# Kernel tuning notes

Hardware: AMD Instinct MI355X
Metric: run time of the kernel (lower is better)

## Reference

```python
import jax, jax.numpy as jnp
import numpy as np

EPS = 1e-12  # torch F.normalize eps


def setup_inputs() -> dict:
    key = jax.random.key(0)
    k1, k2, k3 = jax.random.split(key, 3)
    N, C, H, W, K = 32, 128, 112, 112, 64
    x = jax.random.normal(k1, (N, C, H, W), dtype=jnp.float32)
    conv_w = jax.random.normal(k2, (K, C), dtype=jnp.float32) * 0.05  # 1x1 conv weight, no bias (vladv2=False)
    centroids = jax.random.uniform(k3, (K, C), dtype=jnp.float32)
    return {"x": x, "conv_w": conv_w, "centroids": centroids}


def reference(x, conv_w, centroids):
    N, C = x.shape[:2]
    K = centroids.shape[0]
    xf = x.reshape(N, C, -1)                       # (N, C, S)
    # 1x1 conv == per-pixel linear: (K,C) @ (N,C,S) -> (N,K,S)
    soft_assign = jnp.einsum('kc,ncs->nks', conv_w, xf)
    soft_assign = jax.nn.softmax(soft_assign, axis=1)  # softmax over clusters
    # vlad[n,k,c] = sum_s a[n,k,s] * (x[n,c,s] - cent[k,c])
    vlad = jnp.einsum('nks,ncs->nkc', soft_assign, xf) \
         - soft_assign.sum(axis=-1)[..., None] * centroids[None, :, :]
    # intra-normalize over descriptor dim
    vlad = vlad / jnp.maximum(jnp.linalg.norm(vlad, axis=2, keepdims=True), EPS)
    vlad = vlad.reshape(N, K * C)
    vlad = vlad / jnp.maximum(jnp.linalg.norm(vlad, axis=1, keepdims=True), EPS)
    return vlad
```

## Files before the change

kernel.cpp:

```cpp
#include <hip/hip_runtime.h>

#define NV_N 32
#define NV_C 128
#define NV_K 64
#define NV_S 12544
#define ST 64
#define TILES 14
#define SCHUNK 14
#define XS 72
#define AS 72

typedef short short8 __attribute__((ext_vector_type(8)));
typedef float floatx4 __attribute__((ext_vector_type(4)));

static __device__ __forceinline__ unsigned short f2bf(float f) {
  union { float f; unsigned u; } v; v.f = f;
  unsigned r = v.u + 0x7FFFu + ((v.u >> 16) & 1u);
  return (unsigned short)(r >> 16);
}

static __device__ __forceinline__ short8 pack8(float4 a, float4 b) {
  union { unsigned short us[8]; short8 s; } u;
  u.us[0] = f2bf(a.x); u.us[1] = f2bf(a.y); u.us[2] = f2bf(a.z); u.us[3] = f2bf(a.w);
  u.us[4] = f2bf(b.x); u.us[5] = f2bf(b.y); u.us[6] = f2bf(b.z); u.us[7] = f2bf(b.w);
  return u.s;
}

__global__ __launch_bounds__(256, 2) void netvlad_main(
    const float* __restrict__ x, const float* __restrict__ conv_w,
    float* __restrict__ vlad_ws, float* __restrict__ asum_ws) {
  __shared__ __attribute__((aligned(16))) unsigned short x_lds[2][NV_C * XS];
  __shared__ __attribute__((aligned(16))) unsigned short a_lds[NV_K * AS];
  __shared__ float asum_sh[4][NV_K];

  const int t = threadIdx.x;
  const int n = blockIdx.x / SCHUNK;
  const int chunk = blockIdx.x % SCHUNK;
  const int s_base = chunk * (ST * TILES);
  const int w = t >> 6;
  const int lane = t & 63;
  const int q = lane >> 4;
  const int l = lane & 15;

  const float* __restrict__ xn = x + (size_t)n * NV_C * NV_S;

  short8 wfrag[4][4];
#pragma unroll
  for (int mt = 0; mt < 4; ++mt)
#pragma unroll
    for (int kc = 0; kc < 4; ++kc) {
      const float* wp = conv_w + (mt * 16 + l) * NV_C + kc * 32 + q * 8;
      float4 wa = *(const float4*)wp;
      float4 wb = *(const float4*)(wp + 4);
      wfrag[mt][kc] = pack8(wa, wb);
    }

  floatx4 acc2[4][2];
  float asum_acc[4][4];
#pragma unroll
  for (int mt = 0; mt < 4; ++mt) {
#pragma unroll
    for (int nt = 0; nt < 2; ++nt) acc2[mt][nt] = (floatx4){0.f, 0.f, 0.f, 0.f};
#pragma unroll
    for (int r = 0; r < 4; ++r) asum_acc[mt][r] = 0.f;
  }

  float4 pf[8];

  {
#pragma unroll
    for (int g = 0; g < 4; ++g) {
      int vec2 = t + g * 256; int c = vec2 >> 3; int sv8 = vec2 & 7;
      const float* p = xn + (size_t)c * NV_S + s_base + sv8 * 8;
      pf[2 * g] = *(const float4*)p;
      pf[2 * g + 1] = *(const float4*)(p + 4);
    }
  }

  for (int tt = 0; tt < TILES; ++tt) {
    const int buf = tt & 1;
#pragma unroll
    for (int g = 0; g < 4; ++g) {
      int vec2 = t + g * 256; int c = vec2 >> 3; int sv8 = vec2 & 7;
      *(short8*)&x_lds[buf][c * XS + sv8 * 8] = pack8(pf[2 * g], pf[2 * g + 1]);
    }
    __syncthreads();

    if (tt + 1 < TILES) {
      const int s0n = s_base + (tt + 1) * ST;
#pragma unroll
      for (int g = 0; g < 4; ++g) {
        int vec2 = t + g * 256; int c = vec2 >> 3; int sv8 = vec2 & 7;
        const float* p = xn + (size_t)c * NV_S + s0n + sv8 * 8;
        pf[2 * g] = *(const float4*)p;
        pf[2 * g + 1] = *(const float4*)(p + 4);
      }
    }

    floatx4 acc1[4];
#pragma unroll
    for (int mt = 0; mt < 4; ++mt) acc1[mt] = (floatx4){0.f, 0.f, 0.f, 0.f};
#pragma unroll
    for (int kc = 0; kc < 4; ++kc) {
      short8 bfr;
#pragma unroll
      for (int j = 0; j < 8; ++j)
        bfr[j] = (short)x_lds[buf][(kc * 32 + q * 8 + j) * XS + w * 16 + l];
#pragma unroll
      for (int mt = 0; mt < 4; ++mt)
        acc1[mt] = __builtin_amdgcn_mfma_f32_16x16x32_bf16(wfrag[mt][kc], bfr, acc1[mt], 0, 0, 0);
    }

    {
      float m = -1e30f;
#pragma unroll
      for (int mt = 0; mt < 4; ++mt)
#pragma unroll
        for (int r = 0; r < 4; ++r) m = fmaxf(m, acc1[mt][r]);
      m = fmaxf(m, __shfl_xor(m, 16));
      m = fmaxf(m, __shfl_xor(m, 32));
      float sum = 0.f;
#pragma unroll
      for (int mt = 0; mt < 4; ++mt)
#pragma unroll
        for (int r = 0; r < 4; ++r) {
          float e = __expf(acc1[mt][r] - m);
          acc1[mt][r] = e; sum += e;
        }
      sum += __shfl_xor(sum, 16);
      sum += __shfl_xor(sum, 32);
      const float inv = 1.0f / sum;
#pragma unroll
      for (int mt = 0; mt < 4; ++mt)
#pragma unroll
        for (int r = 0; r < 4; ++r) {
          float a = acc1[mt][r] * inv;
          asum_acc[mt][r] += a;
          a_lds[(mt * 16 + q * 4 + r) * AS + w * 16 + l] = f2bf(a);
        }
    }
    __syncthreads();

#pragma unroll
    for (int sk = 0; sk < 2; ++sk) {
      short8 afr[4];
#pragma unroll
      for (int mt = 0; mt < 4; ++mt)
        afr[mt] = *(const short8*)&a_lds[(mt * 16 + l) * AS + sk * 32 + q * 8];
#pragma unroll
      for (int nt = 0; nt < 2; ++nt) {
        const short8 bfr = *(const short8*)&x_lds[buf][((w * 2 + nt) * 16 + l) * XS + sk * 32 + q * 8];
#pragma unroll
        for (int mt = 0; mt < 4; ++mt)
          acc2[mt][nt] = __builtin_amdgcn_mfma_f32_16x16x32_bf16(afr[mt], bfr, acc2[mt][nt], 0, 0, 0);
      }
    }
  }

#pragma unroll
  for (int mt = 0; mt < 4; ++mt)
#pragma unroll
    for (int r = 0; r < 4; ++r) {
      float v = asum_acc[mt][r];
      v += __shfl_xor(v, 1); v += __shfl_xor(v, 2);
      v += __shfl_xor(v, 4); v += __shfl_xor(v, 8);
      if (l == 0) asum_sh[w][mt * 16 + q * 4 + r] = v;
    }
  __syncthreads();
  if (t < NV_K)
    atomicAdd(asum_ws + (size_t)n * NV_K + t,
              asum_sh[0][t] + asum_sh[1][t] + asum_sh[2][t] + asum_sh[3][t]);

  float* vw = vlad_ws + (size_t)n * (NV_K * NV_C);
#pragma unroll
  for (int mt = 0; mt < 4; ++mt)
#pragma unroll
    for (int nt = 0; nt < 2; ++nt)
#pragma unroll
      for (int r = 0; r < 4; ++r)
        atomicAdd(vw + (mt * 16 + q * 4 + r) * NV_C + (w * 2 + nt) * 16 + l, acc2[mt][nt][r]);
}

__global__ __launch_bounds__(256) void netvlad_finalize(
    const float* __restrict__ vlad_ws, const float* __restrict__ asum_ws,
    const float* __restrict__ cent, float* __restrict__ out) {
  __shared__ float v_lds[NV_K * NV_C];
  __shared__ float red4[256];
  __shared__ float rscale[NV_K];
  __shared__ float gscale_sh;

  const int t = threadIdx.x; const int n = blockIdx.x;
  const float* vw = vlad_ws + (size_t)n * (NV_K * NV_C);

#pragma unroll
  for (int i = 0; i < 8; ++i) {
    int vec = t + i * 256; int k = vec >> 5; int cq = vec & 31;
    float4 ws = *(const float4*)(vw + k * NV_C + cq * 4);
    float4 ce = *(const float4*)(cent + k * NV_C + cq * 4);
    float as = asum_ws[(size_t)n * NV_K + k];
    float4 v;
    v.x = ws.x - as * ce.x; v.y = ws.y - as * ce.y;
    v.z = ws.z - as * ce.z; v.w = ws.w - as * ce.w;
    *(float4*)&v_lds[k * NV_C + cq * 4] = v;
  }
  __syncthreads();

  {
    const int k = t >> 2, part = t & 3;
    const float* row = &v_lds[k * NV_C + part * 32];
    float ss = 0.0f;
#pragma unroll
    for (int c = 0; c < 32; ++c) { float v = row[c]; ss += v * v; }
    red4[t] = ss;
  }
  __syncthreads();
  if (t < NV_K) {
    float ss = red4[t * 4] + red4[t * 4 + 1] + red4[t * 4 + 2] + red4[t * 4 + 3];
    rscale[t] = 1.0f / fmaxf(sqrtf(ss), 1e-12f);
  }
  __syncthreads();

  float gp = 0.0f;
#pragma unroll
  for (int i = 0; i < 8; ++i) {
    int vec = t + i * 256; int k = vec >> 5; int cq = vec & 31;
    float4 v = *(const float4*)&v_lds[k * NV_C + cq * 4];
    float rs = rscale[k];
    gp += (v.x * v.x + v.y * v.y + v.z * v.z + v.w * v.w) * rs * rs;
  }
  red4[t] = gp;
  __syncthreads();
  if (t < 64) {
    float s = red4[t] + red4[t + 64] + red4[t + 128] + red4[t + 192];
#pragma unroll
    for (int o = 32; o > 0; o >>= 1) s += __shfl_down(s, o);
    if (t == 0) gscale_sh = 1.0f / fmaxf(sqrtf(s), 1e-12f);
  }
  __syncthreads();
  const float gs = gscale_sh;

#pragma unroll
  for (int i = 0; i < 8; ++i) {
    int vec = t + i * 256; int k = vec >> 5; int cq = vec & 31;
    float4 v = *(const float4*)&v_lds[k * NV_C + cq * 4];
    const float sc = rscale[k] * gs;
    v.x *= sc; v.y *= sc; v.z *= sc; v.w *= sc;
    *(float4*)(out + (size_t)n * (NV_K * NV_C) + k * NV_C + cq * 4) = v;
  }
}

extern "C" void kernel_launch(void* const* d_in, const int* in_sizes, int n_in,
                              void* d_out, int out_size, void* d_ws, size_t ws_size,
                              hipStream_t stream) {
  (void)in_sizes; (void)n_in; (void)out_size; (void)ws_size;
  const float* x      = (const float*)d_in[0];
  const float* conv_w = (const float*)d_in[1];
  const float* cent   = (const float*)d_in[2];
  float* out = (float*)d_out;

  float* vlad_ws = (float*)d_ws;
  float* asum_ws = vlad_ws + (size_t)NV_N * NV_K * NV_C;
  const size_t zbytes = ((size_t)NV_N * NV_K * NV_C + (size_t)NV_N * NV_K) * sizeof(float);
  hipMemsetAsync(d_ws, 0, zbytes, stream);

  hipLaunchKernelGGL(netvlad_main, dim3(NV_N * SCHUNK), dim3(256), 0, stream,
                     x, conv_w, vlad_ws, asum_ws);
  hipLaunchKernelGGL(netvlad_finalize, dim3(NV_N), dim3(256), 0, stream,
                     vlad_ws, asum_ws, cent, out);
}
```

Baseline: 299.6 us.

## Swizzle x tile in LDS and replace atomics with per-block partials reduced in finalize

The x tile in LDS now uses an XOR-like rotation of 8-element groups by channel, so both MFMA operand reads avoid bank conflicts. Per-chunk global pointers and write offsets are precomputed once instead of each tile. The float atomicAdds into a zeroed workspace are replaced by plain stores of per-block partials, which the finalize kernel sums over the 14 chunks. This also drops the memset. The cost is more workspace traffic in a finalize kernel that runs only 32 blocks.

```diff
diff --git a/kernel.cpp b/kernel.cpp
--- a/kernel.cpp
+++ b/kernel.cpp
@@ -26,9 +26,10 @@
   return u.s;
 }
 
+
 __global__ __launch_bounds__(256, 2) void netvlad_main(
     const float* __restrict__ x, const float* __restrict__ conv_w,
-    float* __restrict__ vlad_ws, float* __restrict__ asum_ws) {
+    float* __restrict__ vlad_part, float* __restrict__ asum_part) {
   __shared__ __attribute__((aligned(16))) unsigned short x_lds[2][NV_C * XS];
   __shared__ __attribute__((aligned(16))) unsigned short a_lds[NV_K * AS];
   __shared__ float asum_sh[4][NV_K];
@@ -65,35 +66,34 @@
     for (int r = 0; r < 4; ++r) asum_acc[mt][r] = 0.f;
   }
 
+  int wroff[4]; const float* gp[4];
+#pragma unroll
+  for (int g = 0; g < 4; ++g) {
+    int vec2 = t + g * 256; int c = vec2 >> 3; int sv8 = vec2 & 7;
+    wroff[g] = c * XS + (((sv8 + (c >> 3)) & 7) << 3);
+    gp[g] = xn + (size_t)c * NV_S + s_base + sv8 * 8;
+  }
+
   float4 pf[8];
-
-  {
-#pragma unroll
-    for (int g = 0; g < 4; ++g) {
-      int vec2 = t + g * 256; int c = vec2 >> 3; int sv8 = vec2 & 7;
-      const float* p = xn + (size_t)c * NV_S + s_base + sv8 * 8;
-      pf[2 * g] = *(const float4*)p;
-      pf[2 * g + 1] = *(const float4*)(p + 4);
-    }
+#pragma unroll
+  for (int g = 0; g < 4; ++g) {
+    pf[2 * g] = *(const float4*)gp[g];
+    pf[2 * g + 1] = *(const float4*)(gp[g] + 4);
   }
 
   for (int tt = 0; tt < TILES; ++tt) {
     const int buf = tt & 1;
 #pragma unroll
-    for (int g = 0; g < 4; ++g) {
-      int vec2 = t + g * 256; int c = vec2 >> 3; int sv8 = vec2 & 7;
-      *(short8*)&x_lds[buf][c * XS + sv8 * 8] = pack8(pf[2 * g], pf[2 * g + 1]);
-    }
+    for (int g = 0; g < 4; ++g)
+      *(short8*)&x_lds[buf][wroff[g]] = pack8(pf[2 * g], pf[2 * g + 1]);
     __syncthreads();
 
     if (tt + 1 < TILES) {
-      const int s0n = s_base + (tt + 1) * ST;
+      const int soff = (tt + 1) * ST;
 #pragma unroll
       for (int g = 0; g < 4; ++g) {
-        int vec2 = t + g * 256; int c = vec2 >> 3; int sv8 = vec2 & 7;
-        const float* p = xn + (size_t)c * NV_S + s0n + sv8 * 8;
-        pf[2 * g] = *(const float4*)p;
-        pf[2 * g + 1] = *(const float4*)(p + 4);
+        pf[2 * g] = *(const float4*)(gp[g] + soff);
+        pf[2 * g + 1] = *(const float4*)(gp[g] + soff + 4);
       }
     }
 
@@ -102,10 +102,11 @@
     for (int mt = 0; mt < 4; ++mt) acc1[mt] = (floatx4){0.f, 0.f, 0.f, 0.f};
 #pragma unroll
     for (int kc = 0; kc < 4; ++kc) {
+      const int gsel = (w * 2 + (l >> 3) + kc * 4 + q) & 7;
       short8 bfr;
 #pragma unroll
       for (int j = 0; j < 8; ++j)
-        bfr[j] = (short)x_lds[buf][(kc * 32 + q * 8 + j) * XS + w * 16 + l];
+        bfr[j] = (short)x_lds[buf][(kc * 32 + q * 8 + j) * XS + (gsel << 3) + (l & 7)];
 #pragma unroll
       for (int mt = 0; mt < 4; ++mt)
         acc1[mt] = __builtin_amdgcn_mfma_f32_16x16x32_bf16(wfrag[mt][kc], bfr, acc1[mt], 0, 0, 0);
@@ -149,7 +150,9 @@
         afr[mt] = *(const short8*)&a_lds[(mt * 16 + l) * AS + sk * 32 + q * 8];
 #pragma unroll
       for (int nt = 0; nt < 2; ++nt) {
-        const short8 bfr = *(const short8*)&x_lds[buf][((w * 2 + nt) * 16 + l) * XS + sk * 32 + q * 8];
+        const int c2 = (w * 2 + nt) * 16 + l;
+        const int gsel2 = (sk * 4 + q + (c2 >> 3)) & 7;
+        const short8 bfr = *(const short8*)&x_lds[buf][c2 * XS + (gsel2 << 3)];
 #pragma unroll
         for (int mt = 0; mt < 4; ++mt)
           acc2[mt][nt] = __builtin_amdgcn_mfma_f32_16x16x32_bf16(afr[mt], bfr, acc2[mt][nt], 0, 0, 0);
@@ -168,39 +171,54 @@
     }
   __syncthreads();
   if (t < NV_K)
-    atomicAdd(asum_ws + (size_t)n * NV_K + t,
-              asum_sh[0][t] + asum_sh[1][t] + asum_sh[2][t] + asum_sh[3][t]);
-
-  float* vw = vlad_ws + (size_t)n * (NV_K * NV_C);
+    asum_part[(size_t)blockIdx.x * NV_K + t] =
+        asum_sh[0][t] + asum_sh[1][t] + asum_sh[2][t] + asum_sh[3][t];
+
+  float* vp = vlad_part + (size_t)blockIdx.x * (NV_K * NV_C);
 #pragma unroll
   for (int mt = 0; mt < 4; ++mt)
 #pragma unroll
     for (int nt = 0; nt < 2; ++nt)
 #pragma unroll
       for (int r = 0; r < 4; ++r)
-        atomicAdd(vw + (mt * 16 + q * 4 + r) * NV_C + (w * 2 + nt) * 16 + l, acc2[mt][nt][r]);
+        vp[(mt * 16 + q * 4 + r) * NV_C + (w * 2 + nt) * 16 + l] = acc2[mt][nt][r];
 }
 
 __global__ __launch_bounds__(256) void netvlad_finalize(
-    const float* __restrict__ vlad_ws, const float* __restrict__ asum_ws,
+    const float* __restrict__ vlad_part, const float* __restrict__ asum_part,
     const float* __restrict__ cent, float* __restrict__ out) {
   __shared__ float v_lds[NV_K * NV_C];
   __shared__ float red4[256];
   __shared__ float rscale[NV_K];
+  __shared__ float asum_tot[NV_K];
   __shared__ float gscale_sh;
 
   const int t = threadIdx.x; const int n = blockIdx.x;
-  const float* vw = vlad_ws + (size_t)n * (NV_K * NV_C);
+  const float* vp = vlad_part + (size_t)n * SCHUNK * (NV_K * NV_C);
+
+  if (t < NV_K) {
+    float s = 0.f;
+#pragma unroll
+    for (int ch = 0; ch < SCHUNK; ++ch)
+      s += asum_part[((size_t)n * SCHUNK + ch) * NV_K + t];
+    asum_tot[t] = s;
+  }
+  __syncthreads();
 
 #pragma unroll
   for (int i = 0; i < 8; ++i) {
     int vec = t + i * 256; int k = vec >> 5; int cq = vec & 31;
-    float4 ws = *(const float4*)(vw + k * NV_C + cq * 4);
+    float ax = 0.f, ay = 0.f, az = 0.f, aw = 0.f;
+#pragma unroll
+    for (int ch = 0; ch < SCHUNK; ++ch) {
+      float4 p = *(const float4*)(vp + (size_t)ch * (NV_K * NV_C) + k * NV_C + cq * 4);
+      ax += p.x; ay += p.y; az += p.z; aw += p.w;
+    }
     float4 ce = *(const float4*)(cent + k * NV_C + cq * 4);
-    float as = asum_ws[(size_t)n * NV_K + k];
+    float as = asum_tot[k];
     float4 v;
-    v.x = ws.x - as * ce.x; v.y = ws.y - as * ce.y;
-    v.z = ws.z - as * ce.z; v.w = ws.w - as * ce.w;
+    v.x = ax - as * ce.x; v.y = ay - as * ce.y;
+    v.z = az - as * ce.z; v.w = aw - as * ce.w;
     *(float4*)&v_lds[k * NV_C + cq * 4] = v;
   }
   __syncthreads();
@@ -258,13 +276,11 @@
   const float* cent   = (const float*)d_in[2];
   float* out = (float*)d_out;
 
-  float* vlad_ws = (float*)d_ws;
-  float* asum_ws = vlad_ws + (size_t)NV_N * NV_K * NV_C;
-  const size_t zbytes = ((size_t)NV_N * NV_K * NV_C + (size_t)NV_N * NV_K) * sizeof(float);
-  hipMemsetAsync(d_ws, 0, zbytes, stream);
+  float* vlad_part = (float*)d_ws;
+  float* asum_part = vlad_part + (size_t)NV_N * SCHUNK * NV_K * NV_C;
 
   hipLaunchKernelGGL(netvlad_main, dim3(NV_N * SCHUNK), dim3(256), 0, stream,
-                     x, conv_w, vlad_ws, asum_ws);
+                     x, conv_w, vlad_part, asum_part);
   hipLaunchKernelGGL(netvlad_finalize, dim3(NV_N), dim3(256), 0, stream,
-                     vlad_ws, asum_ws, cent, out);
-}
+                     vlad_part, asum_part, cent, out);
+}
```

Result: no change. 301.3 us (+0.6%).
